# Kernel optimization log

Measured on AMD Instinct MI355X. Metric: run time of the kernel, lower is better.

The kernel has to match this reference:

```python
import jax, jax.numpy as jnp
import numpy as np

NG, SNG, NS, SNS, NR = 4, 2, 4, 2, 3
NW = 4
STEP = 1 + NG + SNG + NS + SNS + NR  # 16
T, D = 512, 64
MARGIN, ALPHA, BETA, P, R = 1.0, 0.01, 1.0, 0.1, 0.1
KNUM, KMUL = 5, 2.0
GAMMA = 5.0          # soft-dtw gamma
BIG = 1e9            # finite 'inf' so softmin grads stay NaN-free
SIZ = NW * (NW + 1) // 2  # mmds buffer size in the original (zero padded)


def setup_inputs() -> dict:
    key = jax.random.key(0)
    k1, k2 = jax.random.split(key)
    data = jax.random.normal(k1, (NW * STEP, T, D), dtype=jnp.float32)
    lens = jax.random.randint(k2, (NW * STEP,), 64, T + 1, dtype=jnp.int32)
    return {"data": data, "lens": lens}


def _softdtw(Dmat, la, lb):
    """Soft-DTW via anti-diagonal scan. Dmat: (T,T) squared-euclid costs.
    Returns R[la, lb]; DP cells only depend on smaller indices so padding is inert."""
    Tn = Dmat.shape[0]
    idx = jnp.arange(Tn)

    def step(carry, k):
        r2, r1 = carry                      # diagonals k-2 and k-1, indexed by i
        j = k - idx
        valid = (j >= 0) & (j < Tn)
        d = jnp.where(valid, Dmat[idx, jnp.clip(j, 0, Tn - 1)], BIG)
        up = jnp.where(idx > 0, jnp.roll(r1, 1), BIG)     # cell (i-1, j)
        left = r1                                          # cell (i, j-1)
        diag = jnp.where(idx > 0, jnp.roll(r2, 1), BIG)    # cell (i-1, j-1)
        diag = jnp.where((idx == 0) & (k == 0), 0.0, diag)  # R[0,0] = 0 border
        m = jnp.stack([diag, up, left])
        softmin = -GAMMA * jax.nn.logsumexp(-m / GAMMA, axis=0)
        r = jnp.where(valid, d + softmin, BIG)
        return (r1, r), r

    init = (jnp.full((Tn,), BIG, Dmat.dtype), jnp.full((Tn,), BIG, Dmat.dtype))
    _, rows = jax.lax.scan(step, init, jnp.arange(2 * Tn - 1))
    # rows[k, i] = R[i+1, k-i+1]; want R[la, lb] -> k = la+lb-2, i = la-1
    return rows[la + lb - 2, la - 1]


def _mmd(x, y):
    """Multi-kernel Gaussian MMD (DAN-style MMDLoss), n == m."""
    n = x.shape[0]
    total = jnp.concatenate([x, y], axis=0)          # (2n, F)
    sq = jnp.sum(total * total, axis=1)
    l2 = sq[:, None] + sq[None, :] - 2.0 * (total @ total.T)
    ns = total.shape[0]
    bw = jnp.sum(l2) / (ns * ns - ns)
    bw = bw / (KMUL ** (KNUM // 2))
    bws = bw * (KMUL ** jnp.arange(KNUM, dtype=total.dtype))
    kern = jnp.sum(jnp.exp(-l2[None] / bws[:, None, None]), axis=0)
    XX, YY, XY, YX = kern[:n, :n], kern[n:, n:], kern[:n, n:], kern[n:, :n]
    return jnp.mean(XX + YY - XY - YX)


def _forward(data, lens):
    d = data.reshape(NW, STEP, T, D)
    li = lens.reshape(NW, STEP)
    Lf = li.astype(data.dtype)
    anchors = d[:, 0]          # (nw, T, D)
    others = d[:, 1:]          # (nw, 15, T, D)

    # squared-euclidean cost matrices via GEMM: (nw, 15, T, T)
    a2 = jnp.sum(anchors * anchors, -1)                      # (nw, T)
    b2 = jnp.sum(others * others, -1)                        # (nw, 15, T)
    ab = jnp.einsum('wtd,wjsd->wjts', anchors, others)
    cost = a2[:, None, :, None] + b2[:, :, None, :] - 2.0 * ab

    laB = jnp.broadcast_to(li[:, :1], (NW, STEP - 1))
    sdt = jax.vmap(jax.vmap(_softdtw))(cost, laB, li[:, 1:])  # (nw, 15)
    dist = sdt / (Lf[:, :1] + Lf[:, 1:])

    dist_g = dist[:, :NG + SNG]    # genuine + synthetic genuine (6)
    dist_n = dist[:, NG + SNG:]    # skilled + syn skilled + random (9)

    lk = jax.nn.relu(dist_g[:, :, None] + MARGIN - dist_n[:, None, :])
    ca = jnp.mean(dist_g, axis=1)
    cb = jnp.mean(dist_n[:, :5], axis=1)
    intra = jnp.sum(dist_g - ca[:, None], axis=1)
    inter = jax.nn.relu(BETA - jnp.abs(ca - cb))
    nz = jnp.sum(lk != 0, axis=(1, 2))
    lv = jnp.sum(lk, axis=(1, 2)) / (nz + 1).astype(data.dtype)
    total_loss = jnp.mean(lv + intra * P + inter * R)

    # MMD over all (i, j) pairs written by the original loop (i in 0..nw-1,
    # j in 1..nw-1, i != j); buffer zero-padded to SIZ, then max * alpha.
    groups = d[:, :STEP - 5].reshape(NW, STEP - 5, T * D)
    pi = jnp.array([0, 0, 0, 1, 1, 2, 2, 3, 3])
    pj = jnp.array([1, 2, 3, 2, 3, 1, 3, 1, 2])
    mmds = jax.vmap(_mmd)(groups[pi], groups[pj])
    mmds = jnp.concatenate([mmds, jnp.zeros((SIZ - pi.shape[0],), data.dtype)])
    mmd1 = jnp.max(mmds) * ALPHA
    return total_loss + mmd1


def reference(data, lens):
    return _forward(data, lens)
```

## Files before the change

### kernel.cpp

```cpp
#include <hip/hip_runtime.h>
#include <hip/hip_bf16.h>
#include <hip/hip_fp16.h>

#define TT   512
#define DD   64
#define NWK  4
#define STP  16
#define NPJ  15
#define NBLK 60
#define CMAT (TT * TT)
#define CSCALE 0.2885390081777927f
#define USCALE 3.4657359027997265f
#define BIGC   2.885390081777927e8f

#define SA 132

__global__ __launch_bounds__(256) void cost_kernel(const float* __restrict__ data,
                                                   const int* __restrict__ lens,
                                                   __half* __restrict__ cost, int base) {
  int blk = base + blockIdx.z;
  int w = blk / NPJ, j = blk - w * NPJ;
  int la = lens[w * STP];
  int lb = lens[w * STP + 1 + j];
  int ti = blockIdx.y, tj = blockIdx.x;
  if (ti * 128 >= la || tj * 128 >= lb) return;

  __shared__ float As[DD][SA];
  __shared__ float Bs[DD][SA];
  __shared__ float a2[128], b2[128];

  const float* A = data + ((size_t)(w * STP) * TT + (size_t)ti * 128) * DD;
  const float* B = data + ((size_t)(w * STP + 1 + j) * TT + (size_t)tj * 128) * DD;
  int t = threadIdx.x;

  #pragma unroll
  for (int i = 0; i < 8; ++i) {
    int idx = t + i * 256;
    int r = idx & 127;
    int kq = idx >> 7;
    float4 va = *(const float4*)(A + r * DD + kq * 4);
    As[kq * 4 + 0][r] = va.x; As[kq * 4 + 1][r] = va.y;
    As[kq * 4 + 2][r] = va.z; As[kq * 4 + 3][r] = va.w;
    float4 vb = *(const float4*)(B + r * DD + kq * 4);
    Bs[kq * 4 + 0][r] = vb.x; Bs[kq * 4 + 1][r] = vb.y;
    Bs[kq * 4 + 2][r] = vb.z; Bs[kq * 4 + 3][r] = vb.w;
  }
  __syncthreads();
  if (t < 128) {
    float s = 0.f;
    for (int k = 0; k < DD; ++k) { float x = As[k][t]; s += x * x; }
    a2[t] = s;
  } else {
    float s = 0.f;
    for (int k = 0; k < DD; ++k) { float x = Bs[k][t - 128]; s += x * x; }
    b2[t - 128] = s;
  }
  __syncthreads();

  int r0 = (t >> 4) << 2;
  int c0 = (t & 15) << 2;
  float acc[8][8];
  #pragma unroll
  for (int i = 0; i < 8; ++i)
    #pragma unroll
    for (int q = 0; q < 8; ++q) acc[i][q] = 0.f;

  #pragma unroll 2
  for (int k = 0; k < DD; ++k) {
    float4 aL = *(const float4*)&As[k][r0];
    float4 aH = *(const float4*)&As[k][r0 + 64];
    float4 bL = *(const float4*)&Bs[k][c0];
    float4 bH = *(const float4*)&Bs[k][c0 + 64];
    float a[8] = {aL.x, aL.y, aL.z, aL.w, aH.x, aH.y, aH.z, aH.w};
    float b[8] = {bL.x, bL.y, bL.z, bL.w, bH.x, bH.y, bH.z, bH.w};
    #pragma unroll
    for (int i = 0; i < 8; ++i)
      #pragma unroll
      for (int q = 0; q < 8; ++q)
        acc[i][q] += a[i] * b[q];
  }

  __half* Cbase = cost + (size_t)blockIdx.z * CMAT;
  #pragma unroll
  for (int i = 0; i < 8; ++i) {
    int rr = (i < 4) ? (r0 + i) : (r0 + 60 + i);
    float ar = a2[rr];
    __half* Crow = Cbase + (size_t)(ti * 128 + rr) * TT + tj * 128;
    float4 o;
    o.x = (ar + b2[c0 + 0] - 2.f * acc[i][0]) * CSCALE;
    o.y = (ar + b2[c0 + 1] - 2.f * acc[i][1]) * CSCALE;
    o.z = (ar + b2[c0 + 2] - 2.f * acc[i][2]) * CSCALE;
    o.w = (ar + b2[c0 + 3] - 2.f * acc[i][3]) * CSCALE;
    __half2 h01 = __floats2half2_rn(o.x, o.y);
    __half2 h23 = __floats2half2_rn(o.z, o.w);
    uint2 pk; pk.x = *(unsigned*)&h01; pk.y = *(unsigned*)&h23;
    *(uint2*)(Crow + c0) = pk;
    float4 o2;
    o2.x = (ar + b2[c0 + 64] - 2.f * acc[i][4]) * CSCALE;
    o2.y = (ar + b2[c0 + 65] - 2.f * acc[i][5]) * CSCALE;
    o2.z = (ar + b2[c0 + 66] - 2.f * acc[i][6]) * CSCALE;
    o2.w = (ar + b2[c0 + 67] - 2.f * acc[i][7]) * CSCALE;
    __half2 g01 = __floats2half2_rn(o2.x, o2.y);
    __half2 g23 = __floats2half2_rn(o2.z, o2.w);
    uint2 pk2; pk2.x = *(unsigned*)&g01; pk2.y = *(unsigned*)&g23;
    *(uint2*)(Crow + c0 + 64) = pk2;
  }
}

__device__ __forceinline__ float dpcell(float dc, float a, float b, float c) {
  float mn = fminf(fminf(a, b), c);
  float mx = fmaxf(fmaxf(a, b), c);
  float md = __builtin_amdgcn_fmed3f(a, b, c);
  float e = 1.0f + __builtin_amdgcn_exp2f(mn - md) + __builtin_amdgcn_exp2f(mn - mx);
  return dc + mn - __builtin_amdgcn_logf(e);
}

__device__ __forceinline__ float wave_shr1(float x) {
  int xi = __float_as_int(x);
  int r = __builtin_amdgcn_update_dpp(xi, xi, 0x138 , 0xF, 0xF, false);
  return __int_as_float(r);
}

__global__ __launch_bounds__(256) void dp_gram_kernel(const __half* __restrict__ cost,
                                                      const int* __restrict__ lens,
                                                      const float* __restrict__ data,
                                                      float* __restrict__ sdt,
                                                      float* __restrict__ gram,
                                                      int base, int ndp) {
  int bid = blockIdx.x;

  if (bid >= ndp) {
    __shared__ float red[4][16];
    int g = bid - ndp;
    int bx = g / 11, by = g - bx * 11;
    int t = threadIdx.x;
    const float* Ar[4]; const float* Br[4];
    #pragma unroll
    for (int a = 0; a < 4; ++a) {
      int gx = bx * 4 + a;
      Ar[a] = data + (size_t)((gx / 11) * STP + gx % 11) * (TT * DD);
      int gy = by * 4 + a;
      Br[a] = data + (size_t)((gy / 11) * STP + gy % 11) * (TT * DD);
    }
    float acc[4][4];
    #pragma unroll
    for (int a = 0; a < 4; ++a)
      #pragma unroll
      for (int b = 0; b < 4; ++b) acc[a][b] = 0.f;
    for (int k = t * 4; k < TT * DD; k += 1024) {
      float4 av[4], bv[4];
      #pragma unroll
      for (int a = 0; a < 4; ++a) av[a] = *(const float4*)(Ar[a] + k);
      #pragma unroll
      for (int b = 0; b < 4; ++b) bv[b] = *(const float4*)(Br[b] + k);
      #pragma unroll
      for (int a = 0; a < 4; ++a)
        #pragma unroll
        for (int b = 0; b < 4; ++b)
          acc[a][b] += av[a].x * bv[b].x + av[a].y * bv[b].y +
                       av[a].z * bv[b].z + av[a].w * bv[b].w;
    }
    int wave = t >> 6, lane = t & 63;
    #pragma unroll
    for (int a = 0; a < 4; ++a)
      #pragma unroll
      for (int b = 0; b < 4; ++b) {
        float v = acc[a][b];
        for (int off = 32; off > 0; off >>= 1) v += __shfl_down(v, off);
        if (lane == 0) red[wave][a * 4 + b] = v;
      }
    __syncthreads();
    if (t < 16) {
      float v = red[0][t] + red[1][t] + red[2][t] + red[3][t];
      int a = t >> 2, b = t & 3;
      gram[(size_t)(bx * 4 + a) * 44 + by * 4 + b] = v;
    }
    return;
  }

  __shared__ float bufB[3][600];
  __shared__ int flags[4];

  if (threadIdx.x < 4) flags[threadIdx.x] = 0;
  __syncthreads();

  int blk = base + bid;
  int w = blk / NPJ, j = blk - w * NPJ;
  int la = lens[w * STP];
  int lb = lens[w * STP + 1 + j];
  const __half* C = cost + (size_t)bid * CMAT;

  int q = threadIdx.x >> 6, ln = threadIdx.x & 63;
  int c0 = q * 128 + ln * 2;
  const __half* Cp = C + c0;

  int qt = (lb - 1) >> 7;
  int lt = ((lb - 1) >> 1) & 63;
  int par = (lb - 1) & 1;
  int rt = la - 1;
  bool isT = (q == qt) && (ln == lt);

  float U0 = BIGC, U1 = BIGC;
  float NL = BIGC;
  float NLd = (q == 0 && ln == 0) ? 0.0f : BIGC;
  float v1s = BIGC;
  float res = 0.0f;

  int ngrp = (la + 70) >> 3;

  float2 cc[8];
  unsigned cn[8];
  #pragma unroll
  for (int k = 0; k < 8; ++k) {
    int rr = k - ln; rr = rr < 0 ? 0 : (rr > 511 ? 511 : rr);
    __half2 hv = *(const __half2*)(Cp + (size_t)rr * TT);
    cc[k] = __half22float2(hv);
  }
  float bb[8];

  for (int g = 0; g < ngrp; ++g) {
    if (q > 0) {
      int need = 8 * g + 9; if (need > la) need = la;
      while (*(volatile int*)&flags[q - 1] < need) __builtin_amdgcn_s_sleep(2);
      __threadfence_block();
      #pragma unroll
      for (int k = 0; k < 8; ++k) bb[k] = bufB[q - 1][8 * g + 1 + k];
      if (g == 0) {
        float nl0 = bufB[q - 1][0];
        if (ln == 0) NL = nl0;
      }
    }
    #pragma unroll
    for (int k = 0; k < 8; ++k) {
      int rr = 8 * (g + 1) + k - ln; rr = rr < 0 ? 0 : (rr > 511 ? 511 : rr);
      cn[k] = *(const unsigned*)(Cp + (size_t)rr * TT);
    }
    #pragma unroll
    for (int k = 0; k < 8; ++k) {
      int r = 8 * g + k - ln;
      bool act = ((unsigned)r < 512u);
      if (act) {
        float v0 = dpcell(cc[k].x, NLd, U0, NL);
        float v1 = dpcell(cc[k].y, U0, U1, v0);
        if (isT & (r == rt)) res = par ? v1 : v0;
        NLd = NL; U0 = v0; U1 = v1; v1s = v1;
        if (q < 3 && ln == 63) {
          bufB[q][r] = v1;
          if ((r & 7) == 7) {
            __threadfence_block();
            *(volatile int*)&flags[q] = r + 1;
          }
        }
      }
      float nb = wave_shr1(v1s);
      if (ln == 0) nb = (q == 0) ? BIGC : bb[k];
      NL = nb;
    }
    #pragma unroll
    for (int k = 0; k < 8; ++k) {
      __half2 hv = *(__half2*)&cn[k];
      cc[k] = __half22float2(hv);
    }
  }
  if (q < 3 && ln == 63) {
    __threadfence_block();
    *(volatile int*)&flags[q] = 512;
  }
  if (isT) sdt[blk] = res * USCALE;
}

__global__ __launch_bounds__(640) void final_kernel(const float* __restrict__ sdt,
                                                    const int* __restrict__ lens,
                                                    const float* __restrict__ gram,
                                                    float* __restrict__ out) {
  __shared__ float partial[16];
  int t = threadIdx.x, wave = t >> 6, lane = t & 63;
  if (wave < 9) {
    const int piA[9] = {0, 0, 0, 1, 1, 2, 2, 3, 3};
    const int pjA[9] = {1, 2, 3, 2, 3, 1, 3, 1, 2};
    int P = piA[wave], Q = pjA[wave];
    float s1 = 0.f;
    for (int c = lane; c < 484; c += 64) {
      int i = c / 22, jj = c - (c / 22) * 22;
      int gi = (i < 11) ? P * 11 + i : Q * 11 + (i - 11);
      int gj = (jj < 11) ? P * 11 + jj : Q * 11 + (jj - 11);
      s1 += gram[gi * 44 + gi] + gram[gj * 44 + gj] - 2.f * gram[gi * 44 + gj];
    }
    for (int off = 32; off > 0; off >>= 1) s1 += __shfl_down(s1, off);
    s1 = __shfl(s1, 0);
    float bw = s1 / 462.0f * 0.25f;
    float inv[5];
    float b = bw;
    #pragma unroll
    for (int qq = 0; qq < 5; ++qq) { inv[qq] = -1.0f / b; b *= 2.0f; }
    float s2 = 0.f;
    for (int c = lane; c < 484; c += 64) {
      int i = c / 22, jj = c - (c / 22) * 22;
      int gi = (i < 11) ? P * 11 + i : Q * 11 + (i - 11);
      int gj = (jj < 11) ? P * 11 + jj : Q * 11 + (jj - 11);
      float l2 = gram[gi * 44 + gi] + gram[gj * 44 + gj] - 2.f * gram[gi * 44 + gj];
      float kk = 0.f;
      #pragma unroll
      for (int qq = 0; qq < 5; ++qq) kk += __expf(l2 * inv[qq]);
      float sgn = ((i < 11) == (jj < 11)) ? 1.0f : -1.0f;
      s2 += sgn * kk;
    }
    for (int off = 32; off > 0; off >>= 1) s2 += __shfl_down(s2, off);
    if (lane == 0) partial[wave] = s2 / 121.0f;
  } else {
    float term = 0.f;
    if (wave == 9 && lane < 4) {
      int w = lane;
      float L0 = (float)lens[w * STP];
      float dist[15];
      for (int qq = 0; qq < 15; ++qq)
        dist[qq] = sdt[w * NPJ + qq] / (L0 + (float)lens[w * STP + 1 + qq]);
      float ca = 0.f, cb = 0.f;
      for (int a = 0; a < 6; ++a) ca += dist[a];
      ca *= (1.0f / 6.0f);
      for (int bq = 6; bq < 11; ++bq) cb += dist[bq];
      cb *= (1.0f / 5.0f);
      float lksum = 0.f; int nz = 0;
      for (int a = 0; a < 6; ++a)
        for (int bq = 6; bq < 15; ++bq) {
          float x = dist[a] + 1.0f - dist[bq];
          if (x > 0.f) { lksum += x; nz += 1; }
        }
      float intra = 0.f;
      for (int a = 0; a < 6; ++a) intra += dist[a] - ca;
      float inter = fmaxf(0.f, 1.0f - fabsf(ca - cb));
      term = lksum / (float)(nz + 1) + intra * 0.1f + inter * 0.1f;
    }
    if (wave == 9) {
      term += __shfl_down(term, 1);
      term += __shfl_down(term, 2);
      if (lane == 0) partial[9] = term * 0.25f;
    }
  }
  __syncthreads();
  if (t == 0) {
    float mx = 0.0f;
    for (int p = 0; p < 9; ++p) mx = fmaxf(mx, partial[p]);
    out[0] = partial[9] + 0.01f * mx;
  }
}

extern "C" void kernel_launch(void* const* d_in, const int* in_sizes, int n_in,
                              void* d_out, int out_size, void* d_ws, size_t ws_size,
                              hipStream_t stream) {
  const float* data = (const float*)d_in[0];
  const int* lens = (const int*)d_in[1];
  float* out = (float*)d_out;

  float* sdtb  = (float*)d_ws;
  float* gramb = sdtb + 64;
  __half* costb = (__half*)((char*)d_ws + 8192);

  size_t avail = (ws_size > 8192) ? (ws_size - 8192) : 0;
  int chunk = (int)(avail / ((size_t)CMAT * sizeof(__half)));
  if (chunk < 1) chunk = 1;
  if (chunk > NBLK) chunk = NBLK;

  bool first = true;
  for (int base = 0; base < NBLK; base += chunk) {
    int n = NBLK - base;
    if (n > chunk) n = chunk;
    cost_kernel<<<dim3(4, 4, n), 256, 0, stream>>>(data, lens, costb, base);
    int extra = first ? 121 : 0;
    dp_gram_kernel<<<n + extra, 256, 0, stream>>>(costb, lens, data, sdtb, gramb, base, n);
    first = false;
  }
  final_kernel<<<1, 640, 0, stream>>>(sdtb, lens, gramb, out);
}
```

Before: 227.8 us.

## Fuse cost and DP kernels with per-matrix readiness counters

Merges the cost-matrix GEMM blocks into the same launch as the soft-DTW DP and Gram blocks. Each DP block spin-waits on a global atomic counter until all 16 cost tiles for its pair are written, so DP work can start before every cost matrix is finished and one kernel boundary disappears. The wave-to-wave shared-memory handoff now uses s_waitcnt instead of block fences, publishes progress at an earlier row in each group of eight, and sleeps for a shorter time while polling. In exchange it adds a counter-zeroing launch, a larger shared-memory footprint for every block, and relies on DP blocks not starving the cost blocks they wait for.

After: 245.2 us. 7.6% more time.

```diff
diff --git a/kernel.cpp b/kernel.cpp
--- a/kernel.cpp
+++ b/kernel.cpp
@@ -1,5 +1,4 @@
 #include <hip/hip_runtime.h>
-#include <hip/hip_bf16.h>
 #include <hip/hip_fp16.h>
 
 #define TT   512
@@ -14,98 +13,7 @@
 #define BIGC   2.885390081777927e8f
 
 #define SA 132
-
-__global__ __launch_bounds__(256) void cost_kernel(const float* __restrict__ data,
-                                                   const int* __restrict__ lens,
-                                                   __half* __restrict__ cost, int base) {
-  int blk = base + blockIdx.z;
-  int w = blk / NPJ, j = blk - w * NPJ;
-  int la = lens[w * STP];
-  int lb = lens[w * STP + 1 + j];
-  int ti = blockIdx.y, tj = blockIdx.x;
-  if (ti * 128 >= la || tj * 128 >= lb) return;
-
-  __shared__ float As[DD][SA];
-  __shared__ float Bs[DD][SA];
-  __shared__ float a2[128], b2[128];
-
-  const float* A = data + ((size_t)(w * STP) * TT + (size_t)ti * 128) * DD;
-  const float* B = data + ((size_t)(w * STP + 1 + j) * TT + (size_t)tj * 128) * DD;
-  int t = threadIdx.x;
-
-  #pragma unroll
-  for (int i = 0; i < 8; ++i) {
-    int idx = t + i * 256;
-    int r = idx & 127;
-    int kq = idx >> 7;
-    float4 va = *(const float4*)(A + r * DD + kq * 4);
-    As[kq * 4 + 0][r] = va.x; As[kq * 4 + 1][r] = va.y;
-    As[kq * 4 + 2][r] = va.z; As[kq * 4 + 3][r] = va.w;
-    float4 vb = *(const float4*)(B + r * DD + kq * 4);
-    Bs[kq * 4 + 0][r] = vb.x; Bs[kq * 4 + 1][r] = vb.y;
-    Bs[kq * 4 + 2][r] = vb.z; Bs[kq * 4 + 3][r] = vb.w;
-  }
-  __syncthreads();
-  if (t < 128) {
-    float s = 0.f;
-    for (int k = 0; k < DD; ++k) { float x = As[k][t]; s += x * x; }
-    a2[t] = s;
-  } else {
-    float s = 0.f;
-    for (int k = 0; k < DD; ++k) { float x = Bs[k][t - 128]; s += x * x; }
-    b2[t - 128] = s;
-  }
-  __syncthreads();
-
-  int r0 = (t >> 4) << 2;
-  int c0 = (t & 15) << 2;
-  float acc[8][8];
-  #pragma unroll
-  for (int i = 0; i < 8; ++i)
-    #pragma unroll
-    for (int q = 0; q < 8; ++q) acc[i][q] = 0.f;
-
-  #pragma unroll 2
-  for (int k = 0; k < DD; ++k) {
-    float4 aL = *(const float4*)&As[k][r0];
-    float4 aH = *(const float4*)&As[k][r0 + 64];
-    float4 bL = *(const float4*)&Bs[k][c0];
-    float4 bH = *(const float4*)&Bs[k][c0 + 64];
-    float a[8] = {aL.x, aL.y, aL.z, aL.w, aH.x, aH.y, aH.z, aH.w};
-    float b[8] = {bL.x, bL.y, bL.z, bL.w, bH.x, bH.y, bH.z, bH.w};
-    #pragma unroll
-    for (int i = 0; i < 8; ++i)
-      #pragma unroll
-      for (int q = 0; q < 8; ++q)
-        acc[i][q] += a[i] * b[q];
-  }
-
-  __half* Cbase = cost + (size_t)blockIdx.z * CMAT;
-  #pragma unroll
-  for (int i = 0; i < 8; ++i) {
-    int rr = (i < 4) ? (r0 + i) : (r0 + 60 + i);
-    float ar = a2[rr];
-    __half* Crow = Cbase + (size_t)(ti * 128 + rr) * TT + tj * 128;
-    float4 o;
-    o.x = (ar + b2[c0 + 0] - 2.f * acc[i][0]) * CSCALE;
-    o.y = (ar + b2[c0 + 1] - 2.f * acc[i][1]) * CSCALE;
-    o.z = (ar + b2[c0 + 2] - 2.f * acc[i][2]) * CSCALE;
-    o.w = (ar + b2[c0 + 3] - 2.f * acc[i][3]) * CSCALE;
-    __half2 h01 = __floats2half2_rn(o.x, o.y);
-    __half2 h23 = __floats2half2_rn(o.z, o.w);
-    uint2 pk; pk.x = *(unsigned*)&h01; pk.y = *(unsigned*)&h23;
-    *(uint2*)(Crow + c0) = pk;
-    float4 o2;
-    o2.x = (ar + b2[c0 + 64] - 2.f * acc[i][4]) * CSCALE;
-    o2.y = (ar + b2[c0 + 65] - 2.f * acc[i][5]) * CSCALE;
-    o2.z = (ar + b2[c0 + 66] - 2.f * acc[i][6]) * CSCALE;
-    o2.w = (ar + b2[c0 + 67] - 2.f * acc[i][7]) * CSCALE;
-    __half2 g01 = __floats2half2_rn(o2.x, o2.y);
-    __half2 g23 = __floats2half2_rn(o2.z, o2.w);
-    uint2 pk2; pk2.x = *(unsigned*)&g01; pk2.y = *(unsigned*)&g23;
-    *(uint2*)(Crow + c0 + 64) = pk2;
-  }
-}
+#define SMEMSZ (2 * DD * SA * 4 + 1024)
 
 __device__ __forceinline__ float dpcell(float dc, float a, float b, float c) {
   float mn = fminf(fminf(a, b), c);
@@ -121,17 +29,125 @@
   return __int_as_float(r);
 }
 
-__global__ __launch_bounds__(256) void dp_gram_kernel(const __half* __restrict__ cost,
-                                                      const int* __restrict__ lens,
-                                                      const float* __restrict__ data,
-                                                      float* __restrict__ sdt,
-                                                      float* __restrict__ gram,
-                                                      int base, int ndp) {
-  int bid = blockIdx.x;
-
-  if (bid >= ndp) {
-    __shared__ float red[4][16];
-    int g = bid - ndp;
+__global__ __launch_bounds__(64) void zero_kernel(int* __restrict__ cnt) {
+  cnt[threadIdx.x] = 0;
+}
+
+__global__ __launch_bounds__(256) void mega_kernel(const float* __restrict__ data,
+                                                   const int* __restrict__ lens,
+                                                   __half* __restrict__ cost,
+                                                   float* __restrict__ sdt,
+                                                   float* __restrict__ gram,
+                                                   int* __restrict__ cnt,
+                                                   int base, int n, int ng) {
+  __shared__ __align__(16) char smem[SMEMSZ];
+  int b = blockIdx.x;
+
+  if (b >= n + ng) {
+    int cb = b - n - ng;
+    int mloc = cb >> 4, tile = cb & 15;
+    int blk = base + mloc;
+    int w = blk / NPJ, j = blk - w * NPJ;
+    int la = lens[w * STP];
+    int lb = lens[w * STP + 1 + j];
+    int ti = tile >> 2, tj = tile & 3;
+    if (ti * 128 >= la || tj * 128 >= lb) {
+      if (threadIdx.x == 0) atomicAdd(&cnt[mloc], 1);
+      return;
+    }
+
+    float (*As)[SA] = (float(*)[SA])smem;
+    float (*Bs)[SA] = (float(*)[SA])(smem + DD * SA * 4);
+    float* a2 = (float*)(smem + 2 * DD * SA * 4);
+    float* b2 = a2 + 128;
+
+    const float* A = data + ((size_t)(w * STP) * TT + (size_t)ti * 128) * DD;
+    const float* B = data + ((size_t)(w * STP + 1 + j) * TT + (size_t)tj * 128) * DD;
+    int t = threadIdx.x;
+
+    #pragma unroll
+    for (int i = 0; i < 8; ++i) {
+      int idx = t + i * 256;
+      int r = idx & 127;
+      int kq = idx >> 7;
+      float4 va = *(const float4*)(A + r * DD + kq * 4);
+      As[kq * 4 + 0][r] = va.x; As[kq * 4 + 1][r] = va.y;
+      As[kq * 4 + 2][r] = va.z; As[kq * 4 + 3][r] = va.w;
+      float4 vb = *(const float4*)(B + r * DD + kq * 4);
+      Bs[kq * 4 + 0][r] = vb.x; Bs[kq * 4 + 1][r] = vb.y;
+      Bs[kq * 4 + 2][r] = vb.z; Bs[kq * 4 + 3][r] = vb.w;
+    }
+    __syncthreads();
+    if (t < 128) {
+      float s = 0.f;
+      for (int k = 0; k < DD; ++k) { float x = As[k][t]; s += x * x; }
+      a2[t] = s;
+    } else {
+      float s = 0.f;
+      for (int k = 0; k < DD; ++k) { float x = Bs[k][t - 128]; s += x * x; }
+      b2[t - 128] = s;
+    }
+    __syncthreads();
+
+    int r0 = (t >> 4) << 2;
+    int c0 = (t & 15) << 2;
+    float acc[8][8];
+    #pragma unroll
+    for (int i = 0; i < 8; ++i)
+      #pragma unroll
+      for (int q = 0; q < 8; ++q) acc[i][q] = 0.f;
+
+    #pragma unroll 2
+    for (int k = 0; k < DD; ++k) {
+      float4 aL = *(const float4*)&As[k][r0];
+      float4 aH = *(const float4*)&As[k][r0 + 64];
+      float4 bL = *(const float4*)&Bs[k][c0];
+      float4 bH = *(const float4*)&Bs[k][c0 + 64];
+      float a[8] = {aL.x, aL.y, aL.z, aL.w, aH.x, aH.y, aH.z, aH.w};
+      float bq[8] = {bL.x, bL.y, bL.z, bL.w, bH.x, bH.y, bH.z, bH.w};
+      #pragma unroll
+      for (int i = 0; i < 8; ++i)
+        #pragma unroll
+        for (int q = 0; q < 8; ++q)
+          acc[i][q] += a[i] * bq[q];
+    }
+
+    __half* Cbase = cost + (size_t)mloc * CMAT;
+    #pragma unroll
+    for (int i = 0; i < 8; ++i) {
+      int rr = (i < 4) ? (r0 + i) : (r0 + 60 + i);
+      float ar = a2[rr];
+      __half* Crow = Cbase + (size_t)(ti * 128 + rr) * TT + tj * 128;
+      float4 o;
+      o.x = (ar + b2[c0 + 0] - 2.f * acc[i][0]) * CSCALE;
+      o.y = (ar + b2[c0 + 1] - 2.f * acc[i][1]) * CSCALE;
+      o.z = (ar + b2[c0 + 2] - 2.f * acc[i][2]) * CSCALE;
+      o.w = (ar + b2[c0 + 3] - 2.f * acc[i][3]) * CSCALE;
+      __half2 h01 = __floats2half2_rn(o.x, o.y);
+      __half2 h23 = __floats2half2_rn(o.z, o.w);
+      uint2 pk; pk.x = *(unsigned*)&h01; pk.y = *(unsigned*)&h23;
+      *(uint2*)(Crow + c0) = pk;
+      float4 o2;
+      o2.x = (ar + b2[c0 + 64] - 2.f * acc[i][4]) * CSCALE;
+      o2.y = (ar + b2[c0 + 65] - 2.f * acc[i][5]) * CSCALE;
+      o2.z = (ar + b2[c0 + 66] - 2.f * acc[i][6]) * CSCALE;
+      o2.w = (ar + b2[c0 + 67] - 2.f * acc[i][7]) * CSCALE;
+      __half2 g01 = __floats2half2_rn(o2.x, o2.y);
+      __half2 g23 = __floats2half2_rn(o2.z, o2.w);
+      uint2 pk2; pk2.x = *(unsigned*)&g01; pk2.y = *(unsigned*)&g23;
+      *(uint2*)(Crow + c0 + 64) = pk2;
+    }
+    __syncthreads();
+    if (threadIdx.x == 0) {
+      __threadfence();
+      atomicAdd(&cnt[mloc], 1);
+    }
+    return;
+  }
+
+  if (b >= n) {
+    float (*red)[16] = (float(*)[16])smem;
+    int g = b - n;
     int bx = g / 11, by = g - bx * 11;
     int t = threadIdx.x;
     const float* Ar[4]; const float* Br[4];
@@ -146,49 +162,57 @@
     #pragma unroll
     for (int a = 0; a < 4; ++a)
       #pragma unroll
-      for (int b = 0; b < 4; ++b) acc[a][b] = 0.f;
+      for (int bq = 0; bq < 4; ++bq) acc[a][bq] = 0.f;
     for (int k = t * 4; k < TT * DD; k += 1024) {
       float4 av[4], bv[4];
       #pragma unroll
       for (int a = 0; a < 4; ++a) av[a] = *(const float4*)(Ar[a] + k);
       #pragma unroll
-      for (int b = 0; b < 4; ++b) bv[b] = *(const float4*)(Br[b] + k);
+      for (int bq = 0; bq < 4; ++bq) bv[bq] = *(const float4*)(Br[bq] + k);
       #pragma unroll
       for (int a = 0; a < 4; ++a)
         #pragma unroll
-        for (int b = 0; b < 4; ++b)
-          acc[a][b] += av[a].x * bv[b].x + av[a].y * bv[b].y +
-                       av[a].z * bv[b].z + av[a].w * bv[b].w;
+        for (int bq = 0; bq < 4; ++bq)
+          acc[a][bq] += av[a].x * bv[bq].x + av[a].y * bv[bq].y +
+                        av[a].z * bv[bq].z + av[a].w * bv[bq].w;
     }
     int wave = t >> 6, lane = t & 63;
     #pragma unroll
     for (int a = 0; a < 4; ++a)
       #pragma unroll
-      for (int b = 0; b < 4; ++b) {
-        float v = acc[a][b];
+      for (int bq = 0; bq < 4; ++bq) {
+        float v = acc[a][bq];
         for (int off = 32; off > 0; off >>= 1) v += __shfl_down(v, off);
-        if (lane == 0) red[wave][a * 4 + b] = v;
+        if (lane == 0) red[wave][a * 4 + bq] = v;
       }
     __syncthreads();
     if (t < 16) {
       float v = red[0][t] + red[1][t] + red[2][t] + red[3][t];
-      int a = t >> 2, b = t & 3;
-      gram[(size_t)(bx * 4 + a) * 44 + by * 4 + b] = v;
+      int a = t >> 2, bq = t & 3;
+      gram[(size_t)(bx * 4 + a) * 44 + by * 4 + bq] = v;
     }
     return;
   }
 
-  __shared__ float bufB[3][600];
-  __shared__ int flags[4];
+  int mloc = b;
+  if (threadIdx.x == 0) {
+    while (__hip_atomic_load(&cnt[mloc], __ATOMIC_ACQUIRE, __HIP_MEMORY_SCOPE_AGENT) < 16)
+      __builtin_amdgcn_s_sleep(2);
+  }
+  __syncthreads();
+  __threadfence();
+
+  float (*bufB)[600] = (float(*)[600])smem;
+  int* flags = (int*)(smem + 3 * 600 * 4);
 
   if (threadIdx.x < 4) flags[threadIdx.x] = 0;
   __syncthreads();
 
-  int blk = base + bid;
+  int blk = base + mloc;
   int w = blk / NPJ, j = blk - w * NPJ;
   int la = lens[w * STP];
   int lb = lens[w * STP + 1 + j];
-  const __half* C = cost + (size_t)bid * CMAT;
+  const __half* C = cost + (size_t)mloc * CMAT;
 
   int q = threadIdx.x >> 6, ln = threadIdx.x & 63;
   int c0 = q * 128 + ln * 2;
@@ -221,8 +245,8 @@
   for (int g = 0; g < ngrp; ++g) {
     if (q > 0) {
       int need = 8 * g + 9; if (need > la) need = la;
-      while (*(volatile int*)&flags[q - 1] < need) __builtin_amdgcn_s_sleep(2);
-      __threadfence_block();
+      while (*(volatile int*)&flags[q - 1] < need) __builtin_amdgcn_s_sleep(1);
+      asm volatile("s_waitcnt lgkmcnt(0)" ::: "memory");
       #pragma unroll
       for (int k = 0; k < 8; ++k) bb[k] = bufB[q - 1][8 * g + 1 + k];
       if (g == 0) {
@@ -246,8 +270,8 @@
         NLd = NL; U0 = v0; U1 = v1; v1s = v1;
         if (q < 3 && ln == 63) {
           bufB[q][r] = v1;
-          if ((r & 7) == 7) {
-            __threadfence_block();
+          if ((r & 7) == 0) {
+            asm volatile("s_waitcnt lgkmcnt(0)" ::: "memory");
             *(volatile int*)&flags[q] = r + 1;
           }
         }
@@ -263,7 +287,7 @@
     }
   }
   if (q < 3 && ln == 63) {
-    __threadfence_block();
+    asm volatile("s_waitcnt lgkmcnt(0)" ::: "memory");
     *(volatile int*)&flags[q] = 512;
   }
   if (isT) sdt[blk] = res * USCALE;
@@ -354,9 +378,10 @@
 
   float* sdtb  = (float*)d_ws;
   float* gramb = sdtb + 64;
-  __half* costb = (__half*)((char*)d_ws + 8192);
-
-  size_t avail = (ws_size > 8192) ? (ws_size - 8192) : 0;
+  int*   cntb  = (int*)((char*)d_ws + 8192);
+  __half* costh = (__half*)((char*)d_ws + 8448);
+
+  size_t avail = (ws_size > 8448) ? (ws_size - 8448) : 0;
   int chunk = (int)(avail / ((size_t)CMAT * sizeof(__half)));
   if (chunk < 1) chunk = 1;
   if (chunk > NBLK) chunk = NBLK;
@@ -365,9 +390,10 @@
   for (int base = 0; base < NBLK; base += chunk) {
     int n = NBLK - base;
     if (n > chunk) n = chunk;
-    cost_kernel<<<dim3(4, 4, n), 256, 0, stream>>>(data, lens, costb, base);
-    int extra = first ? 121 : 0;
-    dp_gram_kernel<<<n + extra, 256, 0, stream>>>(costb, lens, data, sdtb, gramb, base, n);
+    int ng = first ? 121 : 0;
+    zero_kernel<<<1, 64, 0, stream>>>(cntb);
+    mega_kernel<<<n + ng + 16 * n, 256, 0, stream>>>(data, lens, costh, sdtb, gramb,
+                                                     cntb, base, n, ng);
     first = false;
   }
   final_kernel<<<1, 640, 0, stream>>>(sdtb, lens, gramb, out);
```
